# Kernel optimization log

Hardware: AMD Instinct MI355X
Metric: run time of the kernel (lower is better)

## Reference

```python
import jax, jax.numpy as jnp
import numpy as np
import math

DIM_IN = 512
DIM_OUT = 512
KERNEL = 3
STYLE_DIM = 2 * 128
LIN_SCALE = 1.0 / math.sqrt(STYLE_DIM)      # EqualLinear scale (lr_mul=1)
CONV_SCALE = 1.0 / math.sqrt(DIM_IN * KERNEL ** 2)  # fan_in = dim_in * k**2 (as in source)
PAD = KERNEL // 2


def setup_inputs() -> dict:
    key = jax.random.key(0)
    ks = jax.random.split(key, 5)
    B, T = 16, 2048
    x = jax.random.normal(ks[0], (B, DIM_IN, T), dtype=jnp.float32)
    c_src = jax.random.normal(ks[1], (B, 128), dtype=jnp.float32)
    c_trg = jax.random.normal(ks[2], (B, 128), dtype=jnp.float32)
    style_w = jax.random.normal(ks[3], (DIM_IN, STYLE_DIM), dtype=jnp.float32)
    style_b = jnp.ones((DIM_IN,), dtype=jnp.float32)  # bias_init=1
    weight = jax.random.normal(ks[4], (1, DIM_OUT, DIM_IN, KERNEL), dtype=jnp.float32)
    return {"x": x, "c_src": c_src, "c_trg": c_trg,
            "style_w": style_w, "style_b": style_b, "weight": weight}


def reference(x, c_src, c_trg, style_w, style_b, weight):
    B = x.shape[0]
    # EqualLinear: style code s [B, dim_in]
    c = jnp.concatenate([c_src, c_trg], axis=-1)              # [B, 256]
    s = c @ (style_w * LIN_SCALE).T + style_b                 # [B, dim_in]
    # Modulate: w [B, dim_out, dim_in, k]
    w = CONV_SCALE * weight * s[:, None, :, None]
    # Demodulate over (dim_in, k)
    demod = jax.lax.rsqrt(jnp.sum(w * w, axis=(2, 3)) + 1e-8)  # [B, dim_out]
    w = w * demod[:, :, None, None]
    # Per-sample conv1d, padding 'same' (pad = k//2), vmapped over batch
    def conv1(xi, wi):
        # xi: [dim_in, T], wi: [dim_out, dim_in, k]
        out = jax.lax.conv_general_dilated(
            xi[None], wi, window_strides=(1,), padding=[(PAD, PAD)],
            dimension_numbers=("NCH", "OIH", "NCH"))
        return out[0]                                          # [dim_out, T]
    return jax.vmap(conv1)(x, w)                               # [B, dim_out, T]
```

## Files before the change

### kernel.cpp

```cpp
#include <hip/hip_runtime.h>
#include <cstdint>
#include <cstddef>


#define LIN_SCALE  0.0625f
#define CONV_SCALE 0.014731391f

#define B_   16
#define CIN  512
#define COUT 512
#define T_   2048
#define TP   2050

typedef __bf16 bf16x8 __attribute__((ext_vector_type(8)));
typedef float  f32x4  __attribute__((ext_vector_type(4)));
typedef unsigned short u16x8 __attribute__((ext_vector_type(8)));
typedef unsigned short u16x2 __attribute__((ext_vector_type(2)));

#define AS1 __attribute__((address_space(1)))
#define AS3 __attribute__((address_space(3)))

__device__ inline unsigned short f2bf(float f) {
  __bf16 h = (__bf16)f;
  return __builtin_bit_cast(unsigned short, h);
}

__global__ __launch_bounds__(256) void style_kernel(const float* __restrict__ c_src,
                                                    const float* __restrict__ c_trg,
                                                    const float* __restrict__ sw,
                                                    const float* __restrict__ sb,
                                                    float* __restrict__ s) {
  __shared__ float c[256];
  const int b = blockIdx.y;
  const int tid = threadIdx.x;
  c[tid] = (tid < 128) ? c_src[b * 128 + tid] : c_trg[b * 128 + tid - 128];
  __syncthreads();
  const int w = tid >> 6, lane = tid & 63;
  #pragma unroll
  for (int rr = 0; rr < 16; ++rr) {
    const int i = blockIdx.x * 64 + w * 16 + rr;
    const float* row = sw + (size_t)i * 256;
    float acc = row[lane] * c[lane] + row[lane + 64] * c[lane + 64]
              + row[lane + 128] * c[lane + 128] + row[lane + 192] * c[lane + 192];
    #pragma unroll
    for (int off = 32; off; off >>= 1) acc += __shfl_down(acc, off, 64);
    if (lane == 0) s[b * 512 + i] = acc * LIN_SCALE + sb[i];
  }
}

__global__ __launch_bounds__(256) void modw_kernel(const float* __restrict__ weight,
                                                   const float* __restrict__ s,
                                                   unsigned short* __restrict__ Wm) {
  const int o = blockIdx.x;
  const int tid = threadIdx.x;
  __shared__ float wsh[1536];
  __shared__ float svs[16 * 512];
  __shared__ float partial[16][4];
  __shared__ float demv[16];

  #pragma unroll
  for (int j = tid; j < 1536; j += 256) wsh[j] = weight[(size_t)o * 1536 + j];
  #pragma unroll
  for (int j = tid; j < 16 * 512; j += 256) svs[j] = s[j];
  __syncthreads();

  float wr[6];
  #pragma unroll
  for (int q = 0; q < 6; ++q) wr[q] = wsh[tid * 6 + q] * CONV_SCALE;

  const int lane = tid & 63, w = tid >> 6;
  float ssb[16];
  #pragma unroll
  for (int b = 0; b < 16; ++b) {
    const float s0 = svs[b * 512 + 2 * tid];
    const float s1 = svs[b * 512 + 2 * tid + 1];
    float ss = 0.f;
    #pragma unroll
    for (int q = 0; q < 3; ++q) { float v = wr[q] * s0; ss += v * v; }
    #pragma unroll
    for (int q = 3; q < 6; ++q) { float v = wr[q] * s1; ss += v * v; }
    ssb[b] = ss;
  }
  #pragma unroll
  for (int b = 0; b < 16; ++b) {
    float ss = ssb[b];
    #pragma unroll
    for (int off = 32; off; off >>= 1) ss += __shfl_down(ss, off, 64);
    if (lane == 0) partial[b][w] = ss;
  }
  __syncthreads();
  if (tid < 16)
    demv[tid] = rsqrtf(partial[tid][0] + partial[tid][1] + partial[tid][2] + partial[tid][3] + 1e-8f);
  __syncthreads();

  #pragma unroll
  for (int b = 0; b < 16; ++b) {
    const float dem = demv[b];
    const float s0 = svs[b * 512 + 2 * tid] * dem;
    const float s1 = svs[b * 512 + 2 * tid + 1] * dem;
    #pragma unroll
    for (int k = 0; k < 3; ++k) {
      u16x2 v;
      v.x = f2bf(wr[k] * s0);
      v.y = f2bf(wr[3 + k] * s1);
      *(u16x2*)&Wm[(((size_t)b * 3 + k) * 512 + o) * 512 + 2 * tid] = v;
    }
  }
}

__global__ __launch_bounds__(256) void transpose_kernel(const float* __restrict__ x,
                                                        unsigned short* __restrict__ xT) {
  __shared__ float tile[64][65];
  const int b = blockIdx.z, i0 = blockIdx.y * 64, t0 = blockIdx.x * 64;
  const int tid = threadIdx.x;

  const int lr = tid >> 4;
  const int lc = (tid & 15) * 4;
  const float* xb = x + ((size_t)b * CIN + i0) * T_ + t0;
  #pragma unroll
  for (int p = 0; p < 4; ++p) {
    const int r = p * 16 + lr;
    const float4 v = *(const float4*)(xb + (size_t)r * T_ + lc);
    tile[r][lc + 0] = v.x; tile[r][lc + 1] = v.y;
    tile[r][lc + 2] = v.z; tile[r][lc + 3] = v.w;
  }
  if (blockIdx.x == 0 && tid < 8)
    *(u16x8*)&xT[(size_t)b * TP * CIN + i0 + tid * 8] = (u16x8){0,0,0,0,0,0,0,0};
  if (blockIdx.x == gridDim.x - 1 && tid < 8)
    *(u16x8*)&xT[((size_t)b * TP + TP - 1) * CIN + i0 + tid * 8] = (u16x8){0,0,0,0,0,0,0,0};
  __syncthreads();

  const int st = tid >> 3;
  const int si = (tid & 7) * 8;
  unsigned short* xTb = xT + ((size_t)b * TP + 1 + t0) * CIN + i0;
  #pragma unroll
  for (int p = 0; p < 2; ++p) {
    const int t = p * 32 + st;
    u16x8 v;
    #pragma unroll
    for (int q = 0; q < 8; ++q) v[q] = f2bf(tile[si + q][t]);
    *(u16x8*)&xTb[(size_t)t * CIN + si] = v;
  }
}

#define BM 128
#define BN 128
#define BK 32

__global__ __launch_bounds__(256, 4) void gemm_kernel(const unsigned short* __restrict__ Wm,
                                                      const unsigned short* __restrict__ xT,
                                                      float* __restrict__ out) {
  __shared__ unsigned short lA[3 * 128 * 32];
  __shared__ unsigned short lB[130 * 32];

  const int id  = blockIdx.x;
  const int xcd = id & 7;
  const int j   = id >> 3;
  const int b   = xcd + 8 * (j >> 6);
  const int r   = j & 63;
  const int o0  = (r >> 4) * BM;
  const int t0  = (r & 15) * BN;

  const int tid  = threadIdx.x;
  const int lane = tid & 63;
  const int wid  = tid >> 6;
  const int wm   = (wid & 1) * 64;
  const int wn   = (wid >> 1) * 64;
  const int rl   = lane & 15;
  const int kc   = lane >> 4;

  const unsigned short* gW = Wm + ((size_t)b * 3 * 512 + o0) * 512;
  const unsigned short* gX = xT + ((size_t)b * TP + t0) * CIN;

  f32x4 acc[4][4];
  #pragma unroll
  for (int i = 0; i < 4; ++i)
    #pragma unroll
    for (int jj = 0; jj < 4; ++jj) acc[i][jj] = (f32x4){0.f, 0.f, 0.f, 0.f};

  for (int kk = 0; kk < 16; ++kk) {
    const int i0 = kk * 32;
    __syncthreads();
    #pragma unroll
    for (int q = 0; q < 6; ++q) {
      const int ci  = q * 256 + tid;
      const int row = ci >> 2;
      const int tap = row >> 7;
      const int ar  = row & 127;
      const int gc  = ((ci & 3) ^ ((ar >> 1) & 3)) * 8;
      __builtin_amdgcn_global_load_lds(
          (const AS1 void*)(gW + (size_t)tap * 262144 + (size_t)ar * 512 + i0 + gc),
          (AS3 void*)(&lA[ci * 8]), 16, 0, 0);
    }
    #pragma unroll
    for (int q = 0; q < 2; ++q) {
      const int ci  = q * 256 + tid;
      const int row = ci >> 2;
      const int gc  = ((ci & 3) ^ ((row >> 1) & 3)) * 8;
      __builtin_amdgcn_global_load_lds(
          (const AS1 void*)(gX + (size_t)row * CIN + i0 + gc),
          (AS3 void*)(&lB[ci * 8]), 16, 0, 0);
    }
    if (tid < 8) {
      const int ci  = 512 + tid;
      const int row = ci >> 2;
      const int gc  = ((ci & 3) ^ ((row >> 1) & 3)) * 8;
      __builtin_amdgcn_global_load_lds(
          (const AS1 void*)(gX + (size_t)row * CIN + i0 + gc),
          (AS3 void*)(&lB[ci * 8]), 16, 0, 0);
    }
    __syncthreads();

    #pragma unroll
    for (int tap = 0; tap < 3; ++tap) {
      bf16x8 af[4], bfr[4];
      #pragma unroll
      for (int mi = 0; mi < 4; ++mi) {
        const int ra = wm + mi * 16 + rl;
        af[mi] = *(const bf16x8*)&lA[((tap * 128 + ra) * 4 + (kc ^ ((ra >> 1) & 3))) * 8];
      }
      #pragma unroll
      for (int ni = 0; ni < 4; ++ni) {
        const int rb = wn + ni * 16 + rl + tap;
        bfr[ni] = *(const bf16x8*)&lB[(rb * 4 + (kc ^ ((rb >> 1) & 3))) * 8];
      }
      #pragma unroll
      for (int mi = 0; mi < 4; ++mi)
        #pragma unroll
        for (int ni = 0; ni < 4; ++ni)
          acc[mi][ni] = __builtin_amdgcn_mfma_f32_16x16x32_bf16(af[mi], bfr[ni], acc[mi][ni], 0, 0, 0);
    }
  }

  float* ob = out + ((size_t)b * COUT + o0 + wm) * T_ + t0 + wn;
  const int rrow = (lane >> 4) * 4;
  const int ccol = lane & 15;
  #pragma unroll
  for (int mi = 0; mi < 4; ++mi)
    #pragma unroll
    for (int ni = 0; ni < 4; ++ni)
      #pragma unroll
      for (int rr = 0; rr < 4; ++rr)
        ob[(size_t)(mi * 16 + rrow + rr) * T_ + ni * 16 + ccol] = acc[mi][ni][rr];
}

extern "C" void kernel_launch(void* const* d_in, const int* in_sizes, int n_in,
                              void* d_out, int out_size, void* d_ws, size_t ws_size,
                              hipStream_t stream) {
  const float* x       = (const float*)d_in[0];
  const float* c_src   = (const float*)d_in[1];
  const float* c_trg   = (const float*)d_in[2];
  const float* style_w = (const float*)d_in[3];
  const float* style_b = (const float*)d_in[4];
  const float* weight  = (const float*)d_in[5];
  float* out = (float*)d_out;

  char* ws = (char*)d_ws;
  float* s_buf          = (float*)ws;
  unsigned short* Wm    = (unsigned short*)(ws + 32768);
  unsigned short* xTbuf = (unsigned short*)(ws + 32768 + 25165824);

  style_kernel<<<dim3(8, 16), 256, 0, stream>>>(c_src, c_trg, style_w, style_b, s_buf);
  modw_kernel<<<dim3(COUT), 256, 0, stream>>>(weight, s_buf, Wm);
  transpose_kernel<<<dim3(T_ / 64, CIN / 64, B_), 256, 0, stream>>>(x, xTbuf);
  gemm_kernel<<<dim3(1024), 256, 0, stream>>>(Wm, xTbuf, out);
}
```

Baseline: 197.2 us.

## Double-buffer weight tiles in LDS and load activations directly to registers

Weight tiles are stored in LDS in a fragment-major layout and double-buffered, so the next K-slice is prefetched while the current one feeds the MFMAs. This drops one barrier per iteration. The activation (B) operand no longer goes through LDS: each lane loads its bf16x8 fragments for all three taps straight from global memory. This removes LDS traffic and bank-conflict swizzling, but it adds redundant global loads for the overlapping taps, raises register pressure, and lowers the occupancy hint from 4 to 2.

```diff
diff --git a/kernel.cpp b/kernel.cpp
--- a/kernel.cpp
+++ b/kernel.cpp
@@ -145,13 +145,13 @@
 
 #define BM 128
 #define BN 128
-#define BK 32
-
-__global__ __launch_bounds__(256, 4) void gemm_kernel(const unsigned short* __restrict__ Wm,
+#define AFRAGS 24
+#define ABUF (AFRAGS * 64 * 8)
+
+__global__ __launch_bounds__(256, 2) void gemm_kernel(const unsigned short* __restrict__ Wm,
                                                       const unsigned short* __restrict__ xT,
                                                       float* __restrict__ out) {
-  __shared__ unsigned short lA[3 * 128 * 32];
-  __shared__ unsigned short lB[130 * 32];
+  __shared__ unsigned short lA[2 * ABUF];
 
   const int id  = blockIdx.x;
   const int xcd = id & 7;
@@ -166,11 +166,22 @@
   const int wid  = tid >> 6;
   const int wm   = (wid & 1) * 64;
   const int wn   = (wid >> 1) * 64;
-  const int rl   = lane & 15;
-  const int kc   = lane >> 4;
+  const int ga   = (wid & 1) * 4;
 
   const unsigned short* gW = Wm + ((size_t)b * 3 * 512 + o0) * 512;
-  const unsigned short* gX = xT + ((size_t)b * TP + t0) * CIN;
+  const unsigned short* gX = xT + ((size_t)b * TP + t0 + wn + (lane & 15)) * 512
+                                + ((lane >> 4) * 8);
+
+  int sSrc[6], sDst[6];
+  #pragma unroll
+  for (int q = 0; q < 6; ++q) {
+    const int ci = q * 256 + tid;
+    const int f  = ci >> 6;
+    const int l  = ci & 63;
+    const int tap = f >> 3, g = f & 7;
+    sSrc[q] = tap * 262144 + (g * 16 + (l & 15)) * 512 + ((l >> 4) * 8);
+    sDst[q] = ci * 8;
+  }
 
   f32x4 acc[4][4];
   #pragma unroll
@@ -178,57 +189,44 @@
     #pragma unroll
     for (int jj = 0; jj < 4; ++jj) acc[i][jj] = (f32x4){0.f, 0.f, 0.f, 0.f};
 
+  #pragma unroll
+  for (int q = 0; q < 6; ++q)
+    __builtin_amdgcn_global_load_lds((const AS1 void*)(gW + sSrc[q]),
+                                     (AS3 void*)(&lA[sDst[q]]), 16, 0, 0);
+
   for (int kk = 0; kk < 16; ++kk) {
-    const int i0 = kk * 32;
+    const int i0  = kk * 32;
+    const int cur = (kk & 1) * ABUF;
+    const int nxt = ((kk & 1) ^ 1) * ABUF;
+
     __syncthreads();
-    #pragma unroll
-    for (int q = 0; q < 6; ++q) {
-      const int ci  = q * 256 + tid;
-      const int row = ci >> 2;
-      const int tap = row >> 7;
-      const int ar  = row & 127;
-      const int gc  = ((ci & 3) ^ ((ar >> 1) & 3)) * 8;
-      __builtin_amdgcn_global_load_lds(
-          (const AS1 void*)(gW + (size_t)tap * 262144 + (size_t)ar * 512 + i0 + gc),
-          (AS3 void*)(&lA[ci * 8]), 16, 0, 0);
+
+    if (kk < 15) {
+      const int i0n = i0 + 32;
+      #pragma unroll
+      for (int q = 0; q < 6; ++q)
+        __builtin_amdgcn_global_load_lds((const AS1 void*)(gW + sSrc[q] + i0n),
+                                         (AS3 void*)(&lA[nxt + sDst[q]]), 16, 0, 0);
     }
-    #pragma unroll
-    for (int q = 0; q < 2; ++q) {
-      const int ci  = q * 256 + tid;
-      const int row = ci >> 2;
-      const int gc  = ((ci & 3) ^ ((row >> 1) & 3)) * 8;
-      __builtin_amdgcn_global_load_lds(
-          (const AS1 void*)(gX + (size_t)row * CIN + i0 + gc),
-          (AS3 void*)(&lB[ci * 8]), 16, 0, 0);
-    }
-    if (tid < 8) {
-      const int ci  = 512 + tid;
-      const int row = ci >> 2;
-      const int gc  = ((ci & 3) ^ ((row >> 1) & 3)) * 8;
-      __builtin_amdgcn_global_load_lds(
-          (const AS1 void*)(gX + (size_t)row * CIN + i0 + gc),
-          (AS3 void*)(&lB[ci * 8]), 16, 0, 0);
-    }
-    __syncthreads();
+
+    bf16x8 bfr[3][4];
+    #pragma unroll
+    for (int tap = 0; tap < 3; ++tap)
+      #pragma unroll
+      for (int ni = 0; ni < 4; ++ni)
+        bfr[tap][ni] = *(const bf16x8*)(gX + (size_t)(ni * 16 + tap) * 512 + i0);
 
     #pragma unroll
     for (int tap = 0; tap < 3; ++tap) {
-      bf16x8 af[4], bfr[4];
-      #pragma unroll
-      for (int mi = 0; mi < 4; ++mi) {
-        const int ra = wm + mi * 16 + rl;
-        af[mi] = *(const bf16x8*)&lA[((tap * 128 + ra) * 4 + (kc ^ ((ra >> 1) & 3))) * 8];
-      }
-      #pragma unroll
-      for (int ni = 0; ni < 4; ++ni) {
-        const int rb = wn + ni * 16 + rl + tap;
-        bfr[ni] = *(const bf16x8*)&lB[(rb * 4 + (kc ^ ((rb >> 1) & 3))) * 8];
-      }
+      bf16x8 af[4];
+      #pragma unroll
+      for (int mi = 0; mi < 4; ++mi)
+        af[mi] = *(const bf16x8*)&lA[cur + ((tap * 8 + ga + mi) * 64 + lane) * 8];
       #pragma unroll
       for (int mi = 0; mi < 4; ++mi)
         #pragma unroll
         for (int ni = 0; ni < 4; ++ni)
-          acc[mi][ni] = __builtin_amdgcn_mfma_f32_16x16x32_bf16(af[mi], bfr[ni], acc[mi][ni], 0, 0, 0);
+          acc[mi][ni] = __builtin_amdgcn_mfma_f32_16x16x32_bf16(af[mi], bfr[tap][ni], acc[mi][ni], 0, 0, 0);
     }
   }
 
```

After: 280.9 us. +42.4%, slower.
